# Performance work log

Hardware: AMD Instinct MI355X
Metric: run time of the kernel (lower is better)

Reference implementation:

```python
import jax, jax.numpy as jnp
import numpy as np

N_NODES = 200000
N_EDGES = 3200000
NX = 8
NK = 2


def _l2norm(x, eps=1e-12):
    # F.normalize(x, p=2, dim=-1)
    n = jnp.linalg.norm(x, axis=-1, keepdims=True)
    return x / jnp.maximum(n, eps)


def _aniso_conv(x, src, dst, Kw, n_nodes):
    """For each kernel j: out_j[t] = sum_{e: dst[e]=t} Kw[j,e] * x[src[e]].
    Concatenate over kernels along the feature axis."""
    g = x[src]  # [E, d] gather
    def agg(w):  # w: [E]
        return jax.ops.segment_sum(w[:, None] * g, dst, num_segments=n_nodes)
    out = jax.vmap(agg)(Kw)  # [nk, N, d]
    return jnp.transpose(out, (1, 0, 2)).reshape(n_nodes, -1)  # [N, nk*d]


def setup_inputs() -> dict:
    key = jax.random.key(0)
    ks = jax.random.split(key, 8)
    x = jax.random.normal(ks[0], (N_NODES, NX), dtype=jnp.float32)
    src = jax.random.randint(ks[1], (N_EDGES,), 0, N_NODES, dtype=jnp.int64 if jax.config.jax_enable_x64 else jnp.int32)
    dst = jax.random.randint(ks[2], (N_EDGES,), 0, N_NODES, dtype=src.dtype)
    edge_index = jnp.stack([src, dst], axis=0)
    Kw = jax.random.normal(ks[3], (NK, N_EDGES), dtype=jnp.float32)
    d0, d1 = NX * NK, NX * NK * 2          # 16, 32
    d2 = d1 * NK                            # 64
    hidden, out_ch = 128, 64
    W0 = jax.random.normal(ks[4], (d0, d1), dtype=jnp.float32) / np.sqrt(d0)
    b0 = jnp.zeros((d1,), dtype=jnp.float32)
    W1 = jax.random.normal(ks[5], (d2, hidden), dtype=jnp.float32) / np.sqrt(d2)
    b1 = jnp.zeros((hidden,), dtype=jnp.float32)
    W2 = jax.random.normal(ks[6], (hidden, out_ch), dtype=jnp.float32) / np.sqrt(hidden)
    b2 = jnp.zeros((out_ch,), dtype=jnp.float32)
    return {"x": x, "edge_index": edge_index, "Kw": Kw,
            "W0": W0, "b0": b0, "W1": W1, "b1": b1, "W2": W2, "b2": b2}


def reference(x, edge_index, Kw, W0, b0, W1, b1, W2, b2):
    src, dst = edge_index[0], edge_index[1]
    n = x.shape[0]
    # layer 0: AnisoConv -> single-linear MLP -> L2 normalize
    h = _aniso_conv(x, src, dst, Kw, n)      # [N, 16]
    h = h @ W0 + b0                           # [N, 32]
    h = _l2norm(h)
    # layer 1: AnisoConv -> 2-layer MLP (ReLU between) -> L2 normalize
    h = _aniso_conv(h, src, dst, Kw, n)      # [N, 64]
    h = jax.nn.relu(h @ W1 + b1)             # [N, 128]
    h = h @ W2 + b2                           # [N, 64]
    h = _l2norm(h)
    return h
```

## Files before the change

kernel.cpp:

```cpp
#include <hip/hip_runtime.h>

#define NN 200000
#define NE 3200000
#define NB_SCAN 782
#define NBUCK 196
#define BSHIFT 10
#define BMASK 1023
#define SRCMASK 0x3FFFFu
#define NBLK_A 512
#define EPB (NE / NBLK_A)
#define NPASS 13
#define EMAX 18
#define NT_MLP1 12500

using bf16x8 = __attribute__((ext_vector_type(8))) short;
using f32x4  = __attribute__((ext_vector_type(4))) float;

__device__ __forceinline__ float bflo(unsigned u) { return __uint_as_float(u << 16); }
__device__ __forceinline__ float bfhi(unsigned u) { return __uint_as_float(u & 0xffff0000u); }
__device__ __forceinline__ unsigned short f2bfu(float f) {
  unsigned u = __float_as_uint(f);
  return (unsigned short)((u + 0x7fffu + ((u >> 16) & 1u)) >> 16);
}
__device__ __forceinline__ unsigned pack2(float a, float b) {
  return (unsigned)f2bfu(a) | ((unsigned)f2bfu(b) << 16);
}

__device__ __forceinline__ void acc_edge(uint2 e, uint4 u, float* g0, float* g1) {
  float k0 = bflo(e.y), k1 = bfhi(e.y);
  float v0 = bflo(u.x), v1 = bfhi(u.x);
  float v2 = bflo(u.y), v3 = bfhi(u.y);
  float v4 = bflo(u.z), v5 = bfhi(u.z);
  float v6 = bflo(u.w), v7 = bfhi(u.w);
  g0[0] += k0 * v0; g0[1] += k0 * v1; g0[2] += k0 * v2; g0[3] += k0 * v3;
  g0[4] += k0 * v4; g0[5] += k0 * v5; g0[6] += k0 * v6; g0[7] += k0 * v7;
  g1[0] += k1 * v0; g1[1] += k1 * v1; g1[2] += k1 * v2; g1[3] += k1 * v3;
  g1[4] += k1 * v4; g1[5] += k1 * v5; g1[6] += k1 * v6; g1[7] += k1 * v7;
}


__global__ __launch_bounds__(256) void bhist_kernel(const int* __restrict__ dst,
                                                    int* __restrict__ bhT) {
  __shared__ int h[NBUCK];
  for (int k = threadIdx.x; k < NBUCK; k += 256) h[k] = 0;
  __syncthreads();
  int base = blockIdx.x * EPB;
  for (int i = threadIdx.x; i < EPB; i += 256)
    atomicAdd(&h[dst[base + i] >> BSHIFT], 1);
  __syncthreads();
  for (int k = threadIdx.x; k < NBUCK; k += 256)
    bhT[k * NBLK_A + blockIdx.x] = h[k];
}

__global__ __launch_bounds__(NBLK_A) void bscan_kernel(int* __restrict__ bhT,
                                                       int* __restrict__ btot) {
  __shared__ int s[NBLK_A];
  int b = blockIdx.x;
  int v = bhT[b * NBLK_A + threadIdx.x];
  s[threadIdx.x] = v;
  __syncthreads();
#pragma unroll
  for (int off = 1; off < NBLK_A; off <<= 1) {
    int t = (threadIdx.x >= off) ? s[threadIdx.x - off] : 0;
    __syncthreads();
    s[threadIdx.x] += t;
    __syncthreads();
  }
  bhT[b * NBLK_A + threadIdx.x] = s[threadIdx.x] - v;
  if (threadIdx.x == NBLK_A - 1) btot[b] = s[NBLK_A - 1];
}

__global__ __launch_bounds__(256) void bbase_kernel(const int* __restrict__ btot,
                                                    int* __restrict__ bbase) {
  __shared__ int s[256];
  int v = (threadIdx.x < NBUCK) ? btot[threadIdx.x] : 0;
  s[threadIdx.x] = v;
  __syncthreads();
#pragma unroll
  for (int off = 1; off < 256; off <<= 1) {
    int t = (threadIdx.x >= off) ? s[threadIdx.x - off] : 0;
    __syncthreads();
    s[threadIdx.x] += t;
    __syncthreads();
  }
  if (threadIdx.x < NBUCK) bbase[threadIdx.x] = s[threadIdx.x] - v;
  if (threadIdx.x == NBUCK - 1) bbase[NBUCK] = s[threadIdx.x];
}

__global__ __launch_bounds__(256) void bplace_kernel(
    const int* __restrict__ src, const int* __restrict__ dst,
    const float* __restrict__ kw, const int* __restrict__ bhT,
    const int* __restrict__ bbase, uint2* __restrict__ bsorted) {
  __shared__ uint2 stage[EPB];
  __shared__ unsigned char stageK[EPB];
  __shared__ int h[256];
  __shared__ int sc[256];
  __shared__ int lof[256];
  __shared__ int gof[256];
  __shared__ int cur[256];
  int tid = threadIdx.x, blk = blockIdx.x;
  int base = blk * EPB;

  h[tid] = 0;
  __syncthreads();
  for (int i = tid; i < EPB; i += 256)
    atomicAdd(&h[dst[base + i] >> BSHIFT], 1);
  __syncthreads();
  int v = h[tid];
  sc[tid] = v;
  __syncthreads();
#pragma unroll
  for (int off = 1; off < 256; off <<= 1) {
    int t = (tid >= off) ? sc[tid - off] : 0;
    __syncthreads();
    sc[tid] += t;
    __syncthreads();
  }
  int excl = sc[tid] - v;
  lof[tid] = excl;
  cur[tid] = excl;
  if (tid < NBUCK)
    gof[tid] = bbase[tid] + bhT[tid * NBLK_A + blk] - excl;
  __syncthreads();
  for (int i = tid; i < EPB; i += 256) {
    int e = base + i;
    int d = dst[e];
    int k = d >> BSHIFT;
    int p = atomicAdd(&cur[k], 1);
    uint2 u;
    u.x = (unsigned)src[e] | ((unsigned)(d & BMASK) << 18);
    u.y = pack2(kw[e], kw[NE + e]);
    stage[p] = u;
    stageK[p] = (unsigned char)k;
  }
  __syncthreads();
  for (int i = tid; i < EPB; i += 256) {
    int k = stageK[i];
    bsorted[gof[k] + i] = stage[i];
  }
}


__global__ __launch_bounds__(1024) void nsort_kernel(
    const uint2* __restrict__ bsorted, const int* __restrict__ bbase,
    int* __restrict__ cnt, int* __restrict__ offs, uint2* __restrict__ sedge) {
  __shared__ int h[1024];
  __shared__ int cur[1024];
  int tid = threadIdx.x, b = blockIdx.x;
  h[tid] = 0;
  __syncthreads();
  int r0 = bbase[b], r1 = bbase[b + 1];
  int i0 = r0 + tid;

  uint2 e[EMAX];
#pragma unroll
  for (int j = 0; j < EMAX; ++j) {
    int i = i0 + j * 1024;
    if (i < r1) {
      e[j] = bsorted[i];
      atomicAdd(&h[e[j].x >> 18], 1);
    }
  }
  for (int i = i0 + EMAX * 1024; i < r1; i += 1024)
    atomicAdd(&h[bsorted[i].x >> 18], 1);
  __syncthreads();

  int v = h[tid];
  cur[tid] = v;
  __syncthreads();
  for (int off = 1; off < 1024; off <<= 1) {
    int t = (tid >= off) ? cur[tid - off] : 0;
    __syncthreads();
    cur[tid] += t;
    __syncthreads();
  }
  int excl = r0 + cur[tid] - v;
  int node = b * 1024 + tid;
  if (node < NN) { cnt[node] = v; offs[node] = excl; }
  __syncthreads();
  cur[tid] = excl;
  __syncthreads();

  for (int p = 0; p < NPASS; ++p) {
#pragma unroll
    for (int j = 0; j < EMAX; ++j) {
      int i = i0 + j * 1024;
      if (i < r1) {
        unsigned srcv = e[j].x & SRCMASK;
        if ((int)(srcv >> 14) == p) {
          int pos = atomicAdd(&cur[e[j].x >> 18], 1);
          uint2 w; w.x = srcv; w.y = e[j].y;
          sedge[pos] = w;
        }
      }
    }
    __syncthreads();
  }
  for (int i = i0 + EMAX * 1024; i < r1; i += 1024) {
    uint2 u = bsorted[i];
    int pos = atomicAdd(&cur[u.x >> 18], 1);
    u.x &= SRCMASK;
    sedge[pos] = u;
  }
}


__global__ __launch_bounds__(256) void xcvt_kernel(const float* __restrict__ x,
                                                   unsigned short* __restrict__ xbf) {
  int i = blockIdx.x * 256 + threadIdx.x;
  if (i >= NN) return;
  const float4* xp = reinterpret_cast<const float4*>(x + (size_t)i * 8);
  float4 a = xp[0], b = xp[1];
  uint4 u;
  u.x = pack2(a.x, a.y); u.y = pack2(a.z, a.w);
  u.z = pack2(b.x, b.y); u.w = pack2(b.z, b.w);
  *reinterpret_cast<uint4*>(xbf + (size_t)i * 8) = u;
}


__global__ __launch_bounds__(256) void fused0_kernel(
    const unsigned short* __restrict__ xbf, const int* __restrict__ offs,
    const int* __restrict__ cnt, const uint2* __restrict__ sedge,
    const float* __restrict__ W0, const float* __restrict__ b0,
    unsigned short* __restrict__ h1bf) {
  __shared__ float w0t[32][16];
  __shared__ float b0s[32];
  int tid = threadIdx.x;
  for (int i = tid; i < 16 * 32; i += 256) {
    int k = i >> 5, j = i & 31;
    w0t[j][k] = W0[i];
  }
  if (tid < 32) b0s[tid] = b0[tid];
  __syncthreads();

  int node = blockIdx.x * 256 + tid;
  if (node >= NN) return;

  int start = offs[node];
  int deg = cnt[node];
  float ha[8], hb[8];
#pragma unroll
  for (int k = 0; k < 8; ++k) { ha[k] = 0.f; hb[k] = 0.f; }

  int i = 0;
  for (; i + 4 <= deg; i += 4) {
    uint2 ee[4];
    uint4 uu[4];
#pragma unroll
    for (int j = 0; j < 4; ++j) ee[j] = sedge[start + i + j];
#pragma unroll
    for (int j = 0; j < 4; ++j)
      uu[j] = *reinterpret_cast<const uint4*>(xbf + (size_t)ee[j].x * 8);
#pragma unroll
    for (int j = 0; j < 4; ++j) acc_edge(ee[j], uu[j], ha, hb);
  }
  for (; i < deg; ++i) {
    uint2 e = sedge[start + i];
    uint4 u = *reinterpret_cast<const uint4*>(xbf + (size_t)e.x * 8);
    acc_edge(e, u, ha, hb);
  }

  float o[32];
  float ss = 0.f;
#pragma unroll
  for (int j = 0; j < 32; ++j) {
    float acc = b0s[j];
#pragma unroll
    for (int k = 0; k < 8; ++k) acc += ha[k] * w0t[j][k];
#pragma unroll
    for (int k = 0; k < 8; ++k) acc += hb[k] * w0t[j][8 + k];
    o[j] = acc;
    ss += acc * acc;
  }
  float inv = 1.f / fmaxf(sqrtf(ss), 1e-12f);
  uint4* op = reinterpret_cast<uint4*>(h1bf + (size_t)node * 32);
#pragma unroll
  for (int c = 0; c < 4; ++c) {
    uint4 u;
    u.x = pack2(o[c * 8 + 0] * inv, o[c * 8 + 1] * inv);
    u.y = pack2(o[c * 8 + 2] * inv, o[c * 8 + 3] * inv);
    u.z = pack2(o[c * 8 + 4] * inv, o[c * 8 + 5] * inv);
    u.w = pack2(o[c * 8 + 6] * inv, o[c * 8 + 7] * inv);
    op[c] = u;
  }
}


__global__ __launch_bounds__(256) void gather1_kernel(
    const unsigned short* __restrict__ h1bf, const int* __restrict__ offs,
    const int* __restrict__ cnt, const uint2* __restrict__ sedge,
    unsigned short* __restrict__ gbf) {
  int idx = blockIdx.x * 256 + threadIdx.x;
  int node = idx >> 2, q = idx & 3;
  int start = offs[node];
  int deg = cnt[node];

  float g0[8], g1[8];
#pragma unroll
  for (int k = 0; k < 8; ++k) { g0[k] = 0.f; g1[k] = 0.f; }

  int i = 0;
  for (; i + 8 <= deg; i += 8) {
    uint2 ee[8];
    uint4 uu[8];
#pragma unroll
    for (int j = 0; j < 8; ++j) ee[j] = sedge[start + i + j];
#pragma unroll
    for (int j = 0; j < 8; ++j)
      uu[j] = *reinterpret_cast<const uint4*>(h1bf + (size_t)ee[j].x * 32 + q * 8);
#pragma unroll
    for (int j = 0; j < 8; ++j) acc_edge(ee[j], uu[j], g0, g1);
  }
  for (; i + 4 <= deg; i += 4) {
    uint2 ee[4];
    uint4 uu[4];
#pragma unroll
    for (int j = 0; j < 4; ++j) ee[j] = sedge[start + i + j];
#pragma unroll
    for (int j = 0; j < 4; ++j)
      uu[j] = *reinterpret_cast<const uint4*>(h1bf + (size_t)ee[j].x * 32 + q * 8);
#pragma unroll
    for (int j = 0; j < 4; ++j) acc_edge(ee[j], uu[j], g0, g1);
  }
  for (; i < deg; ++i) {
    uint2 e = sedge[start + i];
    uint4 u = *reinterpret_cast<const uint4*>(h1bf + (size_t)e.x * 32 + q * 8);
    acc_edge(e, u, g0, g1);
  }

  uint4 s0, s1;
  s0.x = pack2(g0[0], g0[1]); s0.y = pack2(g0[2], g0[3]);
  s0.z = pack2(g0[4], g0[5]); s0.w = pack2(g0[6], g0[7]);
  s1.x = pack2(g1[0], g1[1]); s1.y = pack2(g1[2], g1[3]);
  s1.z = pack2(g1[4], g1[5]); s1.w = pack2(g1[6], g1[7]);
  *reinterpret_cast<uint4*>(gbf + (size_t)node * 64 + q * 8) = s0;
  *reinterpret_cast<uint4*>(gbf + (size_t)node * 64 + 32 + q * 8) = s1;
}


__global__ __launch_bounds__(256) void mlp1_kernel(
    const unsigned short* __restrict__ gbf,
    const float* __restrict__ W1, const float* __restrict__ b1,
    const float* __restrict__ W2, const float* __restrict__ b2,
    float* __restrict__ out) {
  __shared__ __align__(16) short hlds[4][16][136];
  int tid = threadIdx.x;
  int wave = tid >> 6, lane = tid & 63;
  int lg = lane >> 4;
  int lr = lane & 15;

  bf16x8 w1f[8][2];
#pragma unroll
  for (int n = 0; n < 8; ++n)
#pragma unroll
    for (int ks = 0; ks < 2; ++ks) {
      bf16x8 f;
#pragma unroll
      for (int i = 0; i < 8; ++i)
        f[i] = (short)f2bfu(W1[(size_t)(ks * 32 + lg * 8 + i) * 128 + n * 16 + lr]);
      w1f[n][ks] = f;
    }
  bf16x8 w2f[4][4];
#pragma unroll
  for (int n2 = 0; n2 < 4; ++n2)
#pragma unroll
    for (int ks = 0; ks < 4; ++ks) {
      bf16x8 f;
#pragma unroll
      for (int i = 0; i < 8; ++i)
        f[i] = (short)f2bfu(W2[(size_t)(ks * 32 + lg * 8 + i) * 64 + n2 * 16 + lr]);
      w2f[n2][ks] = f;
    }
  float b1v[8], b2v[4];
#pragma unroll
  for (int n = 0; n < 8; ++n) b1v[n] = b1[n * 16 + lr];
#pragma unroll
  for (int n2 = 0; n2 < 4; ++n2) b2v[n2] = b2[n2 * 16 + lr];

  for (int tile = blockIdx.x * 4 + wave; tile < NT_MLP1; tile += gridDim.x * 4) {
    int base = tile * 16;
    const bf16x8* grow = reinterpret_cast<const bf16x8*>(gbf + (size_t)(base + lr) * 64);
    bf16x8 a1_0 = grow[lg];
    bf16x8 a1_1 = grow[4 + lg];

#pragma unroll
    for (int n = 0; n < 8; ++n) {
      f32x4 acc = {0.f, 0.f, 0.f, 0.f};
      acc = __builtin_amdgcn_mfma_f32_16x16x32_bf16(a1_0, w1f[n][0], acc, 0, 0, 0);
      acc = __builtin_amdgcn_mfma_f32_16x16x32_bf16(a1_1, w1f[n][1], acc, 0, 0, 0);
#pragma unroll
      for (int q = 0; q < 4; ++q) {
        float v = fmaxf(acc[q] + b1v[n], 0.f);
        hlds[wave][lg * 4 + q][n * 16 + lr] = (short)f2bfu(v);
      }
    }

    bf16x8 a2[4];
#pragma unroll
    for (int ks = 0; ks < 4; ++ks)
      a2[ks] = *reinterpret_cast<const bf16x8*>(&hlds[wave][lr][ks * 32 + lg * 8]);
    f32x4 acc2[4];
#pragma unroll
    for (int n2 = 0; n2 < 4; ++n2) {
      f32x4 a = {0.f, 0.f, 0.f, 0.f};
#pragma unroll
      for (int ks = 0; ks < 4; ++ks)
        a = __builtin_amdgcn_mfma_f32_16x16x32_bf16(a2[ks], w2f[n2][ks], a, 0, 0, 0);
      acc2[n2] = a;
    }

#pragma unroll
    for (int q = 0; q < 4; ++q) {
      float s = 0.f;
#pragma unroll
      for (int n2 = 0; n2 < 4; ++n2) {
        float v = acc2[n2][q] + b2v[n2];
        s += v * v;
      }
      s += __shfl_xor(s, 1); s += __shfl_xor(s, 2);
      s += __shfl_xor(s, 4); s += __shfl_xor(s, 8);
      float inv = 1.f / fmaxf(sqrtf(s), 1e-12f);
      size_t rowoff = (size_t)(base + lg * 4 + q) * 64 + lr;
#pragma unroll
      for (int n2 = 0; n2 < 4; ++n2)
        out[rowoff + n2 * 16] = (acc2[n2][q] + b2v[n2]) * inv;
    }
  }
}


extern "C" void kernel_launch(void* const* d_in, const int* in_sizes, int n_in,
                              void* d_out, int out_size, void* d_ws, size_t ws_size,
                              hipStream_t stream) {
  const float* x  = (const float*)d_in[0];
  const int* ei   = (const int*)d_in[1];
  const float* kw = (const float*)d_in[2];
  const float* W0 = (const float*)d_in[3];
  const float* b0 = (const float*)d_in[4];
  const float* W1 = (const float*)d_in[5];
  const float* b1 = (const float*)d_in[6];
  const float* W2 = (const float*)d_in[7];
  const float* b2 = (const float*)d_in[8];
  float* out = (float*)d_out;

  const int* src = ei;
  const int* dst = ei + NE;

  char* p = (char*)d_ws;
  uint2* bsorted = (uint2*)p;                p += (size_t)NE * 8;
  uint2* sedge   = (uint2*)p;                p += (size_t)NE * 8;
  unsigned short* h1bf = (unsigned short*)p; p += (size_t)NN * 32 * 2;
  unsigned short* xbf  = (unsigned short*)p; p += (size_t)NN * 8 * 2;
  int* bhT   = (int*)p;                      p += (size_t)NBUCK * NBLK_A * 4;
  int* btot  = (int*)p;                      p += (size_t)NBUCK * 4;
  int* bbase = (int*)p;                      p += (size_t)(NBUCK + 1) * 4;
  int* cnt   = (int*)p;                      p += (size_t)NN * 4;
  int* offs  = (int*)p;                      p += (size_t)NN * 4;
  unsigned short* gbf = (unsigned short*)bsorted;

  xcvt_kernel<<<NB_SCAN, 256, 0, stream>>>(x, xbf);

  bhist_kernel<<<NBLK_A, 256, 0, stream>>>(dst, bhT);
  bscan_kernel<<<NBUCK, NBLK_A, 0, stream>>>(bhT, btot);
  bbase_kernel<<<1, 256, 0, stream>>>(btot, bbase);
  bplace_kernel<<<NBLK_A, 256, 0, stream>>>(src, dst, kw, bhT, bbase, bsorted);

  nsort_kernel<<<NBUCK, 1024, 0, stream>>>(bsorted, bbase, cnt, offs, sedge);

  fused0_kernel<<<NB_SCAN, 256, 0, stream>>>(xbf, offs, cnt, sedge, W0, b0, h1bf);
  gather1_kernel<<<(4 * NN) / 256, 256, 0, stream>>>(h1bf, offs, cnt, sedge, gbf);
  mlp1_kernel<<<768, 256, 0, stream>>>(gbf, W1, b1, W2, b2, out);
}
```

Measured before the change: 210.4 us.

## Fuse layer-1 gather with MLP and prepack MLP weights to bf16 fragments

Merges the second-layer neighbour gather and the two-layer MLP into one kernel. Each wave gathers 16 nodes, shuffles the results into MFMA A-fragment layout and runs both matmuls directly, so the intermediate bf16 buffer is never written to or read back from global memory. A one-block kernel pre-converts W1/W2 into fragment-ordered bf16 once per launch, and each wave reloads those fragments from global/L2 instead of converting them from fp32 on every block. The risks are higher register pressure in the fused kernel and weight reload traffic per wave.

After: 231.3 us. 1.1x slower.

```diff
diff --git a/kernel.cpp b/kernel.cpp
--- a/kernel.cpp
+++ b/kernel.cpp
@@ -11,7 +11,6 @@
 #define EPB (NE / NBLK_A)
 #define NPASS 13
 #define EMAX 18
-#define NT_MLP1 12500
 
 using bf16x8 = __attribute__((ext_vector_type(8))) short;
 using f32x4  = __attribute__((ext_vector_type(4))) float;
@@ -95,7 +94,6 @@
   __shared__ unsigned char stageK[EPB];
   __shared__ int h[256];
   __shared__ int sc[256];
-  __shared__ int lof[256];
   __shared__ int gof[256];
   __shared__ int cur[256];
   int tid = threadIdx.x, blk = blockIdx.x;
@@ -117,7 +115,6 @@
     __syncthreads();
   }
   int excl = sc[tid] - v;
-  lof[tid] = excl;
   cur[tid] = excl;
   if (tid < NBUCK)
     gof[tid] = bbase[tid] + bhT[tid * NBLK_A + blk] - excl;
@@ -218,6 +215,31 @@
 }
 
 
+__global__ __launch_bounds__(256) void wpack_kernel(
+    const float* __restrict__ W1, const float* __restrict__ W2,
+    unsigned short* __restrict__ W1p, unsigned short* __restrict__ W2p) {
+  int t = threadIdx.x;
+  {
+    int n = t >> 5, lr = (t >> 1) & 15, ks = t & 1;
+#pragma unroll
+    for (int lg = 0; lg < 4; ++lg)
+#pragma unroll
+      for (int i = 0; i < 8; ++i)
+        W1p[(((n * 16 + lr) * 2 + ks) * 4 + lg) * 8 + i] =
+            f2bfu(W1[(size_t)(ks * 32 + lg * 8 + i) * 128 + n * 16 + lr]);
+  }
+  {
+    int n2 = t >> 6, lr = (t >> 2) & 15, ks = t & 3;
+#pragma unroll
+    for (int lg = 0; lg < 4; ++lg)
+#pragma unroll
+      for (int i = 0; i < 8; ++i)
+        W2p[(((n2 * 16 + lr) * 4 + ks) * 4 + lg) * 8 + i] =
+            f2bfu(W2[(size_t)(ks * 32 + lg * 8 + i) * 64 + n2 * 16 + lr]);
+  }
+}
+
+
 __global__ __launch_bounds__(256) void fused0_kernel(
     const unsigned short* __restrict__ xbf, const int* __restrict__ offs,
     const int* __restrict__ cnt, const uint2* __restrict__ sedge,
@@ -286,12 +308,18 @@
 }
 
 
-__global__ __launch_bounds__(256) void gather1_kernel(
+__global__ __launch_bounds__(256) void gmlp2_kernel(
     const unsigned short* __restrict__ h1bf, const int* __restrict__ offs,
     const int* __restrict__ cnt, const uint2* __restrict__ sedge,
-    unsigned short* __restrict__ gbf) {
-  int idx = blockIdx.x * 256 + threadIdx.x;
-  int node = idx >> 2, q = idx & 3;
+    const unsigned short* __restrict__ W1p, const float* __restrict__ b1,
+    const unsigned short* __restrict__ W2p, const float* __restrict__ b2,
+    float* __restrict__ out) {
+  __shared__ __align__(16) short hl[4][16][136];
+  int tid = threadIdx.x;
+  int wave = tid >> 6, lane = tid & 63;
+
+  int nloc = lane >> 2, q = lane & 3;
+  int node = blockIdx.x * 64 + wave * 16 + nloc;
   int start = offs[node];
   int deg = cnt[node];
 
@@ -328,103 +356,77 @@
     acc_edge(e, u, g0, g1);
   }
 
-  uint4 s0, s1;
-  s0.x = pack2(g0[0], g0[1]); s0.y = pack2(g0[2], g0[3]);
-  s0.z = pack2(g0[4], g0[5]); s0.w = pack2(g0[6], g0[7]);
-  s1.x = pack2(g1[0], g1[1]); s1.y = pack2(g1[2], g1[3]);
-  s1.z = pack2(g1[4], g1[5]); s1.w = pack2(g1[6], g1[7]);
-  *reinterpret_cast<uint4*>(gbf + (size_t)node * 64 + q * 8) = s0;
-  *reinterpret_cast<uint4*>(gbf + (size_t)node * 64 + 32 + q * 8) = s1;
-}
-
-
-__global__ __launch_bounds__(256) void mlp1_kernel(
-    const unsigned short* __restrict__ gbf,
-    const float* __restrict__ W1, const float* __restrict__ b1,
-    const float* __restrict__ W2, const float* __restrict__ b2,
-    float* __restrict__ out) {
-  __shared__ __align__(16) short hlds[4][16][136];
-  int tid = threadIdx.x;
-  int wave = tid >> 6, lane = tid & 63;
-  int lg = lane >> 4;
-  int lr = lane & 15;
-
-  bf16x8 w1f[8][2];
-#pragma unroll
-  for (int n = 0; n < 8; ++n)
-#pragma unroll
-    for (int ks = 0; ks < 2; ++ks) {
-      bf16x8 f;
-#pragma unroll
-      for (int i = 0; i < 8; ++i)
-        f[i] = (short)f2bfu(W1[(size_t)(ks * 32 + lg * 8 + i) * 128 + n * 16 + lr]);
-      w1f[n][ks] = f;
+  unsigned w[8];
+  w[0] = pack2(g0[0], g0[1]); w[1] = pack2(g0[2], g0[3]);
+  w[2] = pack2(g0[4], g0[5]); w[3] = pack2(g0[6], g0[7]);
+  w[4] = pack2(g1[0], g1[1]); w[5] = pack2(g1[2], g1[3]);
+  w[6] = pack2(g1[4], g1[5]); w[7] = pack2(g1[6], g1[7]);
+
+  int srcl = ((lane & 15) << 2) | (lane >> 4);
+  union { unsigned u[4]; bf16x8 v; } fa, fb;
+#pragma unroll
+  for (int j = 0; j < 4; ++j) fa.u[j] = (unsigned)__shfl((int)w[j], srcl);
+#pragma unroll
+  for (int j = 0; j < 4; ++j) fb.u[j] = (unsigned)__shfl((int)w[4 + j], srcl);
+  bf16x8 a1_0 = fa.v;
+  bf16x8 a1_1 = fb.v;
+
+  int lr = lane & 15, lg = lane >> 4;
+  float b1v[8], b2v[4];
+#pragma unroll
+  for (int n = 0; n < 8; ++n) b1v[n] = b1[n * 16 + lr];
+#pragma unroll
+  for (int n2 = 0; n2 < 4; ++n2) b2v[n2] = b2[n2 * 16 + lr];
+
+#pragma unroll
+  for (int n = 0; n < 8; ++n) {
+    bf16x8 w10 = *reinterpret_cast<const bf16x8*>(
+        &W1p[(((n * 16 + lr) * 2 + 0) * 4 + lg) * 8]);
+    bf16x8 w11 = *reinterpret_cast<const bf16x8*>(
+        &W1p[(((n * 16 + lr) * 2 + 1) * 4 + lg) * 8]);
+    f32x4 acc = {0.f, 0.f, 0.f, 0.f};
+    acc = __builtin_amdgcn_mfma_f32_16x16x32_bf16(a1_0, w10, acc, 0, 0, 0);
+    acc = __builtin_amdgcn_mfma_f32_16x16x32_bf16(a1_1, w11, acc, 0, 0, 0);
+#pragma unroll
+    for (int p = 0; p < 4; ++p) {
+      float v = fmaxf(acc[p] + b1v[n], 0.f);
+      hl[wave][lg * 4 + p][n * 16 + lr] = (short)f2bfu(v);
     }
-  bf16x8 w2f[4][4];
-#pragma unroll
-  for (int n2 = 0; n2 < 4; ++n2)
+  }
+
+  bf16x8 a2[4];
+#pragma unroll
+  for (int ks = 0; ks < 4; ++ks)
+    a2[ks] = *reinterpret_cast<const bf16x8*>(&hl[wave][lr][ks * 32 + lg * 8]);
+  f32x4 acc2[4];
+#pragma unroll
+  for (int n2 = 0; n2 < 4; ++n2) {
+    f32x4 a = {0.f, 0.f, 0.f, 0.f};
 #pragma unroll
     for (int ks = 0; ks < 4; ++ks) {
-      bf16x8 f;
-#pragma unroll
-      for (int i = 0; i < 8; ++i)
-        f[i] = (short)f2bfu(W2[(size_t)(ks * 32 + lg * 8 + i) * 64 + n2 * 16 + lr]);
-      w2f[n2][ks] = f;
+      bf16x8 w2 = *reinterpret_cast<const bf16x8*>(
+          &W2p[(((n2 * 16 + lr) * 4 + ks) * 4 + lg) * 8]);
+      a = __builtin_amdgcn_mfma_f32_16x16x32_bf16(a2[ks], w2, a, 0, 0, 0);
     }
-  float b1v[8], b2v[4];
-#pragma unroll
-  for (int n = 0; n < 8; ++n) b1v[n] = b1[n * 16 + lr];
-#pragma unroll
-  for (int n2 = 0; n2 < 4; ++n2) b2v[n2] = b2[n2 * 16 + lr];
-
-  for (int tile = blockIdx.x * 4 + wave; tile < NT_MLP1; tile += gridDim.x * 4) {
-    int base = tile * 16;
-    const bf16x8* grow = reinterpret_cast<const bf16x8*>(gbf + (size_t)(base + lr) * 64);
-    bf16x8 a1_0 = grow[lg];
-    bf16x8 a1_1 = grow[4 + lg];
-
-#pragma unroll
-    for (int n = 0; n < 8; ++n) {
-      f32x4 acc = {0.f, 0.f, 0.f, 0.f};
-      acc = __builtin_amdgcn_mfma_f32_16x16x32_bf16(a1_0, w1f[n][0], acc, 0, 0, 0);
-      acc = __builtin_amdgcn_mfma_f32_16x16x32_bf16(a1_1, w1f[n][1], acc, 0, 0, 0);
-#pragma unroll
-      for (int q = 0; q < 4; ++q) {
-        float v = fmaxf(acc[q] + b1v[n], 0.f);
-        hlds[wave][lg * 4 + q][n * 16 + lr] = (short)f2bfu(v);
-      }
+    acc2[n2] = a;
+  }
+
+  int base = blockIdx.x * 64 + wave * 16;
+#pragma unroll
+  for (int p = 0; p < 4; ++p) {
+    float s = 0.f;
+#pragma unroll
+    for (int n2 = 0; n2 < 4; ++n2) {
+      float v = acc2[n2][p] + b2v[n2];
+      s += v * v;
     }
-
-    bf16x8 a2[4];
-#pragma unroll
-    for (int ks = 0; ks < 4; ++ks)
-      a2[ks] = *reinterpret_cast<const bf16x8*>(&hlds[wave][lr][ks * 32 + lg * 8]);
-    f32x4 acc2[4];
-#pragma unroll
-    for (int n2 = 0; n2 < 4; ++n2) {
-      f32x4 a = {0.f, 0.f, 0.f, 0.f};
-#pragma unroll
-      for (int ks = 0; ks < 4; ++ks)
-        a = __builtin_amdgcn_mfma_f32_16x16x32_bf16(a2[ks], w2f[n2][ks], a, 0, 0, 0);
-      acc2[n2] = a;
-    }
-
-#pragma unroll
-    for (int q = 0; q < 4; ++q) {
-      float s = 0.f;
-#pragma unroll
-      for (int n2 = 0; n2 < 4; ++n2) {
-        float v = acc2[n2][q] + b2v[n2];
-        s += v * v;
-      }
-      s += __shfl_xor(s, 1); s += __shfl_xor(s, 2);
-      s += __shfl_xor(s, 4); s += __shfl_xor(s, 8);
-      float inv = 1.f / fmaxf(sqrtf(s), 1e-12f);
-      size_t rowoff = (size_t)(base + lg * 4 + q) * 64 + lr;
-#pragma unroll
-      for (int n2 = 0; n2 < 4; ++n2)
-        out[rowoff + n2 * 16] = (acc2[n2][q] + b2v[n2]) * inv;
-    }
+    s += __shfl_xor(s, 1); s += __shfl_xor(s, 2);
+    s += __shfl_xor(s, 4); s += __shfl_xor(s, 8);
+    float inv = 1.f / fmaxf(sqrtf(s), 1e-12f);
+    size_t rowoff = (size_t)(base + lg * 4 + p) * 64 + lr;
+#pragma unroll
+    for (int n2 = 0; n2 < 4; ++n2)
+      out[rowoff + n2 * 16] = (acc2[n2][p] + b2v[n2]) * inv;
   }
 }
 
@@ -456,8 +458,10 @@
   int* bbase = (int*)p;                      p += (size_t)(NBUCK + 1) * 4;
   int* cnt   = (int*)p;                      p += (size_t)NN * 4;
   int* offs  = (int*)p;                      p += (size_t)NN * 4;
-  unsigned short* gbf = (unsigned short*)bsorted;
-
+  unsigned short* W1p = (unsigned short*)p;  p += (size_t)8192 * 2;
+  unsigned short* W2p = (unsigned short*)p;  p += (size_t)8192 * 2;
+
+  wpack_kernel<<<1, 256, 0, stream>>>(W1, W2, W1p, W2p);
   xcvt_kernel<<<NB_SCAN, 256, 0, stream>>>(x, xbf);
 
   bhist_kernel<<<NBLK_A, 256, 0, stream>>>(dst, bhT);
@@ -468,6 +472,6 @@
   nsort_kernel<<<NBUCK, 1024, 0, stream>>>(bsorted, bbase, cnt, offs, sedge);
 
   fused0_kernel<<<NB_SCAN, 256, 0, stream>>>(xbf, offs, cnt, sedge, W0, b0, h1bf);
-  gather1_kernel<<<(4 * NN) / 256, 256, 0, stream>>>(h1bf, offs, cnt, sedge, gbf);
-  mlp1_kernel<<<768, 256, 0, stream>>>(gbf, W1, b1, W2, b2, out);
-}
+  gmlp2_kernel<<<NN / 64, 256, 0, stream>>>(h1bf, offs, cnt, sedge,
+                                            W1p, b1, W2p, b2, out);
+}
```
